# Optimization experiments

Hardware: AMD Instinct MI355X
Metric: run time of the kernel (lower is better)

Reference implementation:

```python
import jax, jax.numpy as jnp
import numpy as np

N_NODES = 50000
N_EDGES = 800000
D_FEAT = 128
HIDDEN = 128
OUT = 64
HEADS = 4


def setup_inputs() -> dict:
    key = jax.random.key(0)
    ks = jax.random.split(key, 12)
    s_in = 1.0 / np.sqrt(D_FEAT)
    s_h = 1.0 / np.sqrt(HIDDEN)
    x = jax.random.normal(ks[0], (N_NODES, D_FEAT), dtype=jnp.float32)
    edge_index = jax.random.randint(ks[1], (2, N_EDGES), 0, N_NODES, dtype=jnp.int32)
    return {
        "x": x,
        "edge_index": edge_index,
        # SAGEConv params: lin_l (aggregated neighbors), lin_r (root), bias
        "W_l": jax.random.normal(ks[2], (D_FEAT, HIDDEN), dtype=jnp.float32) * s_in,
        "W_r": jax.random.normal(ks[3], (D_FEAT, HIDDEN), dtype=jnp.float32) * s_in,
        "b_sage": jnp.zeros((HIDDEN,), dtype=jnp.float32),
        # GATConv params: lin_src, lin_dst (heads*hidden each), att vectors, bias
        "W_src": jax.random.normal(ks[4], (HIDDEN, HEADS * HIDDEN), dtype=jnp.float32) * s_h,
        "W_dst": jax.random.normal(ks[5], (HIDDEN, HEADS * HIDDEN), dtype=jnp.float32) * s_h,
        "att_src": jax.random.normal(ks[6], (HEADS, HIDDEN), dtype=jnp.float32) * s_h,
        "att_dst": jax.random.normal(ks[7], (HEADS, HIDDEN), dtype=jnp.float32) * s_h,
        "b_gat": jnp.zeros((HIDDEN,), dtype=jnp.float32),
        # Final Linear
        "W_lin": jax.random.normal(ks[8], (HIDDEN, OUT), dtype=jnp.float32) * s_h,
        "b_lin": jnp.zeros((OUT,), dtype=jnp.float32),
    }


def reference(x, edge_index, W_l, W_r, b_sage, W_src, W_dst, att_src, att_dst, b_gat, W_lin, b_lin):
    N = x.shape[0]
    src = edge_index[0]
    dst = edge_index[1]

    # ---- SAGEConv (mean aggregation): out = lin_l(mean_j x_j) + lin_r(x_i) + b ----
    agg = jax.ops.segment_sum(x[src], dst, num_segments=N)          # [N, d]
    cnt = jax.ops.segment_sum(jnp.ones_like(dst, dtype=x.dtype), dst, num_segments=N)
    mean_nbr = agg / jnp.maximum(cnt, 1.0)[:, None]
    h = mean_nbr @ W_l + x @ W_r + b_sage                           # [N, H*... no: [N, hidden]
    h = jax.nn.relu(h)

    # ---- GATConv (heads=4, concat=False -> mean over heads) ----
    H, C = att_src.shape
    hs = (h @ W_src).reshape(N, H, C)                               # source-transformed [N, H, C]
    hd = (h @ W_dst).reshape(N, H, C)                               # dest-transformed   [N, H, C]
    a_s = jnp.einsum('nhc,hc->nh', hs, att_src)                     # [N, H]
    a_d = jnp.einsum('nhc,hc->nh', hd, att_dst)                     # [N, H]
    e = jax.nn.leaky_relu(a_s[src] + a_d[dst], negative_slope=0.2)  # [E, H]
    # edge softmax over incoming edges per destination node
    e_max = jax.ops.segment_max(e, dst, num_segments=N)             # [N, H]
    e_exp = jnp.exp(e - e_max[dst])                                 # [E, H]
    denom = jax.ops.segment_sum(e_exp, dst, num_segments=N)         # [N, H]
    alpha = e_exp / denom[dst]                                      # [E, H]
    msg = hs[src] * alpha[:, :, None]                               # [E, H, C]
    out = jax.ops.segment_sum(msg, dst, num_segments=N)             # [N, H, C]
    out = out.mean(axis=1) + b_gat                                  # concat=False: avg heads
    out = jax.nn.relu(out)

    # ---- final Linear ----
    return out @ W_lin + b_lin
```

## Files before the change

### kernel.cpp

```cpp
#include <hip/hip_runtime.h>

#define D 128
#define HEADS 4

typedef __attribute__((ext_vector_type(8))) short short8;
typedef __attribute__((ext_vector_type(4))) float f32x4;

static __device__ __forceinline__ float leaky(float v) { return v > 0.f ? v : 0.2f * v; }

static __device__ __forceinline__ float2 bf2_to_f2(unsigned int u) {
    float2 r;
    union { unsigned int i; float f; } a, b;
    a.i = (u & 0xffffu) << 16;
    b.i = u & 0xffff0000u;
    r.x = a.f; r.y = b.f;
    return r;
}
static __device__ __forceinline__ float bf_to_f(unsigned short s) {
    union { unsigned int i; float f; } a;
    a.i = ((unsigned int)s) << 16;
    return a.f;
}
static __device__ __forceinline__ unsigned short f2bf(float f) {
    union { float f; unsigned int i; } v; v.f = f;
    unsigned int u = v.i;
    unsigned int r = (u + 0x7fffu + ((u >> 16) & 1u)) >> 16;
    return (unsigned short)r;
}

#define CPAD 16
#define HIST_BLOCKS 128
#define PREP_CNT 107520
#define MAXBUCK 2048
#define CH 8192

__global__ __launch_bounds__(256) void k_early(const float* __restrict__ x,
                                               const int* __restrict__ ei, int E, int npairs,
                                               const float* __restrict__ Wl, const float* __restrict__ Wr,
                                               const float* __restrict__ Wsrc, const float* __restrict__ Wlin,
                                               const float* __restrict__ Wdst,
                                               const float* __restrict__ atts, const float* __restrict__ attd,
                                               unsigned short* __restrict__ Bh,
                                               unsigned short* __restrict__ Bg,
                                               unsigned short* __restrict__ Bf,
                                               float* __restrict__ wsd,
                                               unsigned int* __restrict__ xb,
                                               int* __restrict__ bhist) {
    __shared__ int sh[MAXBUCK];
    int gb = blockIdx.x, t = threadIdx.x;
    if (gb < HIST_BLOCKS) {
        for (int i = t; i < MAXBUCK; i += 256) sh[i] = 0;
        __syncthreads();
        for (int i = gb * 256 + t; i < E; i += HIST_BLOCKS * 256)
            atomicAdd(&sh[ei[E + i] >> 5], 1);
        __syncthreads();
        for (int i = t; i < MAXBUCK; i += 256) if (sh[i]) atomicAdd(&bhist[i * CPAD], sh[i]);
        return;
    }
    int i = (gb - HIST_BLOCKS) * 256 + t;
    if (i < 32768) {
        int idx = i;
        int j = idx & 7, n16 = (idx >> 3) & 15, quad = (idx >> 7) & 3, rest = idx >> 9;
        int nc = rest & 7, kb = rest >> 3;
        int kk = kb * 32 + quad * 8 + j;
        int n = nc * 16 + n16;
        float v = (kk < 128) ? Wl[kk * 128 + n] : Wr[(kk - 128) * 128 + n];
        Bh[idx] = f2bf(v);
    } else if (i < 32768 + 65536) {
        int idx = i - 32768;
        int j = idx & 7, n16 = (idx >> 3) & 15, quad = (idx >> 7) & 3, rest = idx >> 9;
        int nc = rest & 7, kb = rest >> 3;
        int kk = kb * 32 + quad * 8 + j;
        int n = nc * 16 + n16;
        float v = Wsrc[(kk & 127) * 512 + (kk >> 7) * 128 + n];
        Bg[idx] = f2bf(v);
    } else if (i < 32768 + 65536 + 8192) {
        int idx = i - 98304;
        int j = idx & 7, n16 = (idx >> 3) & 15, quad = (idx >> 7) & 3, rest = idx >> 9;
        int nc = rest & 3, kb = rest >> 2;
        int kk = kb * 32 + quad * 8 + j;
        int n = nc * 16 + n16;
        Bf[idx] = f2bf(Wlin[kk * 64 + n]);
    } else if (i < PREP_CNT) {
        int tt = i - 106496;
        int k = tt >> 3, o = tt & 7;
        int hh = o & 3;
        const float* W = (o < 4) ? Wsrc : Wdst;
        const float* att = (o < 4) ? atts : attd;
        float acc = 0.f;
        for (int c = 0; c < 128; c++) acc += W[k * 512 + hh * 128 + c] * att[hh * 128 + c];
        wsd[k * 8 + o] = acc;
    } else {
        int p = i - PREP_CNT;
        if (p < npairs) {
            float2 v = *(const float2*)(x + (size_t)p * 2);
            xb[p] = (unsigned int)f2bf(v.x) | ((unsigned int)f2bf(v.y) << 16);
        }
    }
}

__global__ __launch_bounds__(256) void k_bscan(const int* __restrict__ bhist, int nbuck, int E,
                                               int* __restrict__ bbase, int* __restrict__ bcur,
                                               int* __restrict__ rowptr, int N) {
    __shared__ int ssum[256];
    int t = threadIdx.x;
    int base = t * 8;
    int v[8]; int s = 0;
    #pragma unroll
    for (int j = 0; j < 8; j++) {
        int idx = base + j;
        v[j] = (idx < nbuck) ? bhist[idx * CPAD] : 0;
        s += v[j];
    }
    ssum[t] = s;
    __syncthreads();
    for (int o = 1; o < 256; o <<= 1) {
        int tv = (t >= o) ? ssum[t - o] : 0;
        __syncthreads();
        ssum[t] += tv;
        __syncthreads();
    }
    int run = ssum[t] - s;
    #pragma unroll
    for (int j = 0; j < 8; j++) {
        int idx = base + j;
        if (idx < nbuck) { bbase[idx] = run; bcur[idx * CPAD] = run; }
        run += v[j];
    }
    if (t == 0) { bbase[nbuck] = E; rowptr[N] = E; }
}

__global__ __launch_bounds__(256) void k_scatter1(const int* __restrict__ ei, int E, int nbuck,
                                                  int* __restrict__ bcur,
                                                  unsigned int* __restrict__ ebuf) {
    __shared__ unsigned int sval[CH];
    __shared__ unsigned short soff[CH];
    __shared__ int cnt[MAXBUCK];
    __shared__ int gbase[MAXBUCK];
    int t = threadIdx.x;
    int c0 = blockIdx.x * CH;
    int ecnt = E - c0; if (ecnt > CH) ecnt = CH;
    for (int i = t; i < MAXBUCK; i += 256) cnt[i] = 0;
    __syncthreads();
    for (int i = t; i < ecnt; i += 256) {
        int s = ei[c0 + i], d = ei[E + c0 + i];
        int b = d >> 5;
        soff[i] = (unsigned short)atomicAdd(&cnt[b], 1);
        sval[i] = (unsigned int)s | ((unsigned int)(d & 31) << 16) | ((unsigned int)b << 21);
    }
    __syncthreads();
    for (int b = t; b < nbuck; b += 256)
        if (cnt[b]) gbase[b] = atomicAdd(&bcur[b * CPAD], cnt[b]);
    __syncthreads();
    for (int i = t; i < ecnt; i += 256) {
        unsigned int v = sval[i];
        int b = v >> 21;
        ebuf[gbase[b] + soff[i]] = v & 0x1fffffu;
    }
}

#define BCAP 1024
__global__ __launch_bounds__(256) void k_build_sage(const unsigned int* __restrict__ ebuf,
                                                    const int* __restrict__ bbase,
                                                    const unsigned int* __restrict__ xb,
                                                    int* __restrict__ csr,
                                                    int* __restrict__ rowptr,
                                                    unsigned int* __restrict__ meanb, int N) {
    __shared__ int cnt[32];
    __shared__ int excl[33];
    __shared__ unsigned char off[BCAP];
    __shared__ unsigned int rawv[BCAP];
    __shared__ int sorted[BCAP];
    int b = blockIdx.x, t = threadIdx.x;
    int e0 = bbase[b], e1 = bbase[b + 1];
    int ecnt = e1 - e0;
    if (ecnt > BCAP) ecnt = BCAP;
    if (t < 32) cnt[t] = 0;
    __syncthreads();
    for (int i = t; i < ecnt; i += 256) {
        unsigned int p = ebuf[e0 + i];
        rawv[i] = p;
        off[i] = (unsigned char)atomicAdd(&cnt[(p >> 16) & 31], 1);
    }
    __syncthreads();
    if (t == 0) {
        int run = 0;
        #pragma unroll
        for (int j = 0; j < 32; j++) { excl[j] = run; run += cnt[j]; }
        excl[32] = run;
    }
    __syncthreads();
    for (int i = t; i < ecnt; i += 256) {
        unsigned int p = rawv[i];
        int d = (p >> 16) & 31;
        sorted[excl[d] + off[i]] = (int)(p & 0xffffu);
    }
    __syncthreads();
    int nb0 = b << 5;
    if (t < 32 && nb0 + t < N) rowptr[nb0 + t] = e0 + excl[t];
    for (int i = t; i < ecnt; i += 256) csr[e0 + i] = sorted[i];
    int wv = t >> 6, lane = t & 63;
    for (int k = 0; k < 8; k++) {
        int local = wv * 8 + k;
        int node = nb0 + local;
        if (node >= N) continue;
        int le0 = excl[local], le1 = excl[local + 1];
        float ax = 0.f, ay = 0.f;
        int e = le0;
        for (; e + 3 < le1; e += 4) {
            int s0 = sorted[e], s1 = sorted[e + 1], s2 = sorted[e + 2], s3 = sorted[e + 3];
            unsigned int u0 = xb[(size_t)s0 * 64 + lane];
            unsigned int u1 = xb[(size_t)s1 * 64 + lane];
            unsigned int u2 = xb[(size_t)s2 * 64 + lane];
            unsigned int u3 = xb[(size_t)s3 * 64 + lane];
            float2 v0 = bf2_to_f2(u0), v1 = bf2_to_f2(u1), v2 = bf2_to_f2(u2), v3 = bf2_to_f2(u3);
            ax += (v0.x + v1.x) + (v2.x + v3.x);
            ay += (v0.y + v1.y) + (v2.y + v3.y);
        }
        for (; e < le1; e++) {
            float2 v0 = bf2_to_f2(xb[(size_t)sorted[e] * 64 + lane]);
            ax += v0.x; ay += v0.y;
        }
        int dg = le1 - le0;
        float inv = 1.0f / (float)(dg > 0 ? dg : 1);
        unsigned int o = (unsigned int)f2bf(ax * inv) | ((unsigned int)f2bf(ay * inv) << 16);
        __builtin_nontemporal_store(o, meanb + (size_t)node * 64 + lane);
    }
}

__global__ __launch_bounds__(256) void k_mfma_h(const unsigned short* __restrict__ A0,
                                                const unsigned short* __restrict__ A1,
                                                const unsigned short* __restrict__ Bp,
                                                const float* __restrict__ bias,
                                                const float* __restrict__ wsd,
                                                unsigned short* __restrict__ outb,
                                                float* __restrict__ a_s,
                                                float* __restrict__ a_d, int M) {
    const int NC = 8;
    __shared__ unsigned short sH[64][136];
    __shared__ float swsd[1024];
    int tid = threadIdx.x;
    int wave = tid >> 6;
    int lane = tid & 63;
    int row0 = blockIdx.x * 64 + wave * 16;
    int n16 = lane & 15, quad = lane >> 4;
    int arow = row0 + n16;
    int arowc = arow < M ? arow : 0;
    for (int i = tid; i < 1024; i += 256) swsd[i] = wsd[i];
    f32x4 acc[NC];
    #pragma unroll
    for (int i = 0; i < NC; i++) acc[i] = (f32x4){0.f, 0.f, 0.f, 0.f};
    #pragma unroll
    for (int kb = 0; kb < 8; kb++) {
        const unsigned short* ap = (kb < 4)
            ? (A0 + (size_t)arowc * 128 + kb * 32 + quad * 8)
            : (A1 + (size_t)arowc * 128 + (kb - 4) * 32 + quad * 8);
        short8 af = *(const short8*)ap;
        #pragma unroll
        for (int nc = 0; nc < NC; nc++) {
            short8 bf = *(const short8*)(Bp + ((((size_t)(kb * NC + nc) * 4 + quad) * 16 + n16) << 3));
            acc[nc] = __builtin_amdgcn_mfma_f32_16x16x32_bf16(af, bf, acc[nc], 0, 0, 0);
        }
    }
    int orow = row0 + quad * 4;
    int lrow = wave * 16 + quad * 4;
    #pragma unroll
    for (int r = 0; r < 4; r++) {
        int m = orow + r;
        #pragma unroll
        for (int nc = 0; nc < NC; nc++) {
            int col = nc * 16 + n16;
            float v = fmaxf(acc[nc][r] + bias[col], 0.f);
            unsigned short bv = f2bf(v);
            sH[lrow + r][col] = bv;
            if (m < M) outb[(size_t)m * 128 + col] = bv;
        }
    }
    __syncthreads();
    #pragma unroll
    for (int j = tid; j < 512; j += 256) {
        int m = j >> 3, o = j & 7;
        float accd = 0.f;
        #pragma unroll 4
        for (int k = 0; k < 128; k++)
            accd += bf_to_f(sH[m][k]) * swsd[k * 8 + o];
        int n = blockIdx.x * 64 + m;
        if (n < M) {
            if (o < 4) a_s[n * 4 + o] = accd;
            else       a_d[n * 4 + (o - 4)] = accd;
        }
    }
}

#define EDGE_CAP 192
__global__ __launch_bounds__(256) void k_gat_agg(const int* __restrict__ rowptr,
                                                 const int* __restrict__ csr,
                                                 const unsigned int* __restrict__ hb,
                                                 const float* __restrict__ a_s,
                                                 const float* __restrict__ a_d,
                                                 unsigned int* __restrict__ aggb, int N) {
    __shared__ int   sSrc[4][EDGE_CAP];
    __shared__ float sAl[4][EDGE_CAP * 4];
    int wv = threadIdx.x >> 6;
    int lane = threadIdx.x & 63;
    int n = blockIdx.x * 4 + wv;
    bool active = n < N;
    int e0 = 0, deg = 0;
    float4 ad = {0.f, 0.f, 0.f, 0.f};
    if (active) {
        e0 = rowptr[n];
        deg = rowptr[n + 1] - e0;
        ad = *(const float4*)(a_d + (size_t)n * 4);
    }
    f32x4 psum = {0.f, 0.f, 0.f, 0.f};
    for (int base = 0; base < deg; base += 64) {
        int i = base + lane;
        if (i < deg) {
            int s = csr[e0 + i];
            float4 as = *(const float4*)(a_s + (size_t)s * 4);
            f32x4 w;
            w.x = __expf(leaky(as.x + ad.x));
            w.y = __expf(leaky(as.y + ad.y));
            w.z = __expf(leaky(as.z + ad.z));
            w.w = __expf(leaky(as.w + ad.w));
            psum += w;
            if (i < EDGE_CAP) {
                sSrc[wv][i] = s;
                *(f32x4*)&sAl[wv][i * 4] = w;
            }
        }
    }
    #pragma unroll
    for (int o = 32; o; o >>= 1) {
        psum.x += __shfl_xor(psum.x, o);
        psum.y += __shfl_xor(psum.y, o);
        psum.z += __shfl_xor(psum.z, o);
        psum.w += __shfl_xor(psum.w, o);
    }
    f32x4 inv;
    inv.x = psum.x > 0.f ? 0.25f / psum.x : 0.f;
    inv.y = psum.y > 0.f ? 0.25f / psum.y : 0.f;
    inv.z = psum.z > 0.f ? 0.25f / psum.z : 0.f;
    inv.w = psum.w > 0.f ? 0.25f / psum.w : 0.f;
    int capdeg = deg < EDGE_CAP ? deg : EDGE_CAP;
    for (int base = 0; base < capdeg; base += 64) {
        int i = base + lane;
        if (i < capdeg) {
            f32x4 w = *(f32x4*)&sAl[wv][i * 4];
            w *= inv;
            *(f32x4*)&sAl[wv][i * 4] = w;
        }
    }
    __syncthreads();
    float2 ac0 = {0, 0}, ac1 = {0, 0}, ac2 = {0, 0}, ac3 = {0, 0};
    int e = 0;
    for (; e + 3 < capdeg; e += 4) {
        int s0 = sSrc[wv][e], s1 = sSrc[wv][e + 1], s2 = sSrc[wv][e + 2], s3 = sSrc[wv][e + 3];
        f32x4 w0 = *(const f32x4*)&sAl[wv][e * 4];
        f32x4 w1 = *(const f32x4*)&sAl[wv][e * 4 + 4];
        f32x4 w2 = *(const f32x4*)&sAl[wv][e * 4 + 8];
        f32x4 w3 = *(const f32x4*)&sAl[wv][e * 4 + 12];
        unsigned int u0 = hb[(size_t)s0 * 64 + lane];
        unsigned int u1 = hb[(size_t)s1 * 64 + lane];
        unsigned int u2 = hb[(size_t)s2 * 64 + lane];
        unsigned int u3 = hb[(size_t)s3 * 64 + lane];
        float2 v0 = bf2_to_f2(u0), v1 = bf2_to_f2(u1), v2 = bf2_to_f2(u2), v3 = bf2_to_f2(u3);
        ac0.x += w0.x * v0.x + w1.x * v1.x + w2.x * v2.x + w3.x * v3.x;
        ac0.y += w0.x * v0.y + w1.x * v1.y + w2.x * v2.y + w3.x * v3.y;
        ac1.x += w0.y * v0.x + w1.y * v1.x + w2.y * v2.x + w3.y * v3.x;
        ac1.y += w0.y * v0.y + w1.y * v1.y + w2.y * v2.y + w3.y * v3.y;
        ac2.x += w0.z * v0.x + w1.z * v1.x + w2.z * v2.x + w3.z * v3.x;
        ac2.y += w0.z * v0.y + w1.z * v1.y + w2.z * v2.y + w3.z * v3.y;
        ac3.x += w0.w * v0.x + w1.w * v1.x + w2.w * v2.x + w3.w * v3.x;
        ac3.y += w0.w * v0.y + w1.w * v1.y + w2.w * v2.y + w3.w * v3.y;
    }
    for (; e < capdeg; e++) {
        int s0 = sSrc[wv][e];
        f32x4 w0 = *(const f32x4*)&sAl[wv][e * 4];
        unsigned int u0 = hb[(size_t)s0 * 64 + lane];
        float2 v0 = bf2_to_f2(u0);
        ac0.x += w0.x * v0.x; ac0.y += w0.x * v0.y;
        ac1.x += w0.y * v0.x; ac1.y += w0.y * v0.y;
        ac2.x += w0.z * v0.x; ac2.y += w0.z * v0.y;
        ac3.x += w0.w * v0.x; ac3.y += w0.w * v0.y;
    }
    for (int i = EDGE_CAP; i < deg; i++) {
        int s = csr[e0 + i];
        float4 as = *(const float4*)(a_s + (size_t)s * 4);
        f32x4 w;
        w.x = __expf(leaky(as.x + ad.x)) * inv.x;
        w.y = __expf(leaky(as.y + ad.y)) * inv.y;
        w.z = __expf(leaky(as.z + ad.z)) * inv.z;
        w.w = __expf(leaky(as.w + ad.w)) * inv.w;
        float2 v0 = bf2_to_f2(hb[(size_t)s * 64 + lane]);
        ac0.x += w.x * v0.x; ac0.y += w.x * v0.y;
        ac1.x += w.y * v0.x; ac1.y += w.y * v0.y;
        ac2.x += w.z * v0.x; ac2.y += w.z * v0.y;
        ac3.x += w.w * v0.x; ac3.y += w.w * v0.y;
    }
    if (!active) return;
    unsigned int* rowu = aggb + (size_t)n * 256 + lane;
    unsigned int o0 = (unsigned int)f2bf(ac0.x) | ((unsigned int)f2bf(ac0.y) << 16);
    unsigned int o1 = (unsigned int)f2bf(ac1.x) | ((unsigned int)f2bf(ac1.y) << 16);
    unsigned int o2 = (unsigned int)f2bf(ac2.x) | ((unsigned int)f2bf(ac2.y) << 16);
    unsigned int o3 = (unsigned int)f2bf(ac3.x) | ((unsigned int)f2bf(ac3.y) << 16);
    __builtin_nontemporal_store(o0, rowu + 0);
    __builtin_nontemporal_store(o1, rowu + 64);
    __builtin_nontemporal_store(o2, rowu + 128);
    __builtin_nontemporal_store(o3, rowu + 192);
}

__global__ __launch_bounds__(256) void k_mfma_tail(const unsigned short* __restrict__ aggb,
                                                   const unsigned short* __restrict__ Bg,
                                                   const float* __restrict__ bg,
                                                   const unsigned short* __restrict__ Bf,
                                                   const float* __restrict__ bl,
                                                   float* __restrict__ out, int M) {
    __shared__ unsigned short sG[64][136];
    int wave = threadIdx.x >> 6;
    int lane = threadIdx.x & 63;
    int row0 = blockIdx.x * 64 + wave * 16;
    int n16 = lane & 15, quad = lane >> 4;
    {
        int arow = row0 + n16;
        int arowc = arow < M ? arow : 0;
        const unsigned short* ap = aggb + (size_t)arowc * 512 + quad * 8;
        f32x4 acc[8];
        #pragma unroll
        for (int i = 0; i < 8; i++) acc[i] = (f32x4){0.f, 0.f, 0.f, 0.f};
        #pragma unroll
        for (int kb = 0; kb < 16; kb++) {
            short8 af = *(const short8*)(ap + kb * 32);
            #pragma unroll
            for (int nc = 0; nc < 8; nc++) {
                short8 bf = *(const short8*)(Bg + ((((size_t)(kb * 8 + nc) * 4 + quad) * 16 + n16) << 3));
                acc[nc] = __builtin_amdgcn_mfma_f32_16x16x32_bf16(af, bf, acc[nc], 0, 0, 0);
            }
        }
        int lrow = wave * 16 + quad * 4;
        #pragma unroll
        for (int r = 0; r < 4; r++) {
            #pragma unroll
            for (int nc = 0; nc < 8; nc++) {
                int col = nc * 16 + n16;
                sG[lrow + r][col] = f2bf(fmaxf(acc[nc][r] + bg[col], 0.f));
            }
        }
    }
    __syncthreads();
    {
        f32x4 acc[4];
        #pragma unroll
        for (int i = 0; i < 4; i++) acc[i] = (f32x4){0.f, 0.f, 0.f, 0.f};
        #pragma unroll
        for (int kb = 0; kb < 4; kb++) {
            short8 af = *(const short8*)&sG[wave * 16 + n16][kb * 32 + quad * 8];
            #pragma unroll
            for (int nc = 0; nc < 4; nc++) {
                short8 bf = *(const short8*)(Bf + ((((size_t)(kb * 4 + nc) * 4 + quad) * 16 + n16) << 3));
                acc[nc] = __builtin_amdgcn_mfma_f32_16x16x32_bf16(af, bf, acc[nc], 0, 0, 0);
            }
        }
        int orow = row0 + quad * 4;
        #pragma unroll
        for (int r = 0; r < 4; r++) {
            int m = orow + r;
            if (m < M) {
                #pragma unroll
                for (int nc = 0; nc < 4; nc++) {
                    int col = nc * 16 + n16;
                    out[(size_t)m * 64 + col] = acc[nc][r] + bl[col];
                }
            }
        }
    }
}

extern "C" void kernel_launch(void* const* d_in, const int* in_sizes, int n_in,
                              void* d_out, int out_size, void* d_ws, size_t ws_size,
                              hipStream_t stream) {
    const float* x    = (const float*)d_in[0];
    const int*   ei   = (const int*)d_in[1];
    const float* Wl   = (const float*)d_in[2];
    const float* Wr   = (const float*)d_in[3];
    const float* bs   = (const float*)d_in[4];
    const float* Wsrc = (const float*)d_in[5];
    const float* Wdst = (const float*)d_in[6];
    const float* atts = (const float*)d_in[7];
    const float* attd = (const float*)d_in[8];
    const float* bg   = (const float*)d_in[9];
    const float* Wlin = (const float*)d_in[10];
    const float* bl   = (const float*)d_in[11];
    int N = in_sizes[0] / D;
    int E = in_sizes[1] / 2;
    int nbuck = (N + 31) >> 5;
    int npairs = N * 64;

    char* w = (char*)d_ws;
    auto alloc = [&](size_t bytes) {
        char* p = w;
        w += (bytes + 255) & ~(size_t)255;
        return p;
    };
    unsigned int* xb     = (unsigned int*)alloc((size_t)N * 256);
    unsigned int* meanb  = (unsigned int*)alloc((size_t)N * 256);
    unsigned int* hb     = (unsigned int*)alloc((size_t)N * 256);
    unsigned int* aggb   = (unsigned int*)alloc((size_t)N * 1024);
    unsigned short* Bh   = (unsigned short*)alloc(65536 * 2);
    unsigned short* Bg   = (unsigned short*)alloc(65536 * 2);
    unsigned short* Bf   = (unsigned short*)alloc(8192 * 2);
    float* a_s           = (float*)alloc((size_t)N * 16);
    float* a_d           = (float*)alloc((size_t)N * 16);
    float* wsd           = (float*)alloc(1024 * 4);
    int* rowptr          = (int*)alloc((size_t)(N + 64) * 4);
    int* bhist           = (int*)alloc((size_t)MAXBUCK * CPAD * 4);
    int* bbase           = (int*)alloc((size_t)(MAXBUCK + 1) * 4);
    int* bcur            = (int*)alloc((size_t)MAXBUCK * CPAD * 4);
    unsigned int* ebuf   = (unsigned int*)alloc((size_t)E * 4);
    int* csr             = (int*)alloc((size_t)E * 4);
    (void)ws_size; (void)n_in; (void)out_size;

    hipMemsetAsync(bhist, 0, (size_t)MAXBUCK * CPAD * 4, stream);

    int workBlocks = (PREP_CNT + npairs + 255) / 256;
    k_early<<<HIST_BLOCKS + workBlocks, 256, 0, stream>>>(x, ei, E, npairs,
                                                          Wl, Wr, Wsrc, Wlin, Wdst, atts, attd,
                                                          Bh, Bg, Bf, wsd, xb, bhist);
    k_bscan<<<1, 256, 0, stream>>>(bhist, nbuck, E, bbase, bcur, rowptr, N);
    k_scatter1<<<(E + CH - 1) / CH, 256, 0, stream>>>(ei, E, nbuck, bcur, ebuf);
    k_build_sage<<<nbuck, 256, 0, stream>>>(ebuf, bbase, xb, csr, rowptr, meanb, N);

    k_mfma_h<<<(N + 63) / 64, 256, 0, stream>>>((const unsigned short*)meanb,
                                                (const unsigned short*)xb, Bh, bs, wsd,
                                                (unsigned short*)hb, a_s, a_d, N);
    k_gat_agg<<<(N + 3) / 4, 256, 0, stream>>>(rowptr, csr, hb, a_s, a_d, aggb, N);
    k_mfma_tail<<<(N + 63) / 64, 256, 0, stream>>>((const unsigned short*)aggb, Bg, bg,
                                                   Bf, bl, (float*)d_out, N);
}
```

Baseline: 270.0 us.

## Replace bucket histogram and scan with fixed-capacity bucket slots; widen GAT gather

Each destination bucket now gets a fixed slot of 1024 edges, so the scatter kernel writes to `b<<10` plus an atomic offset. This removes the histogram pass over edges in `k_early` and the single-block scan kernel. Row extents become explicit `rowptr`/`rowend` arrays instead of a prefix-summed `rowptr`. The GAT aggregation stores precomputed byte offsets in shared memory, unrolls the gather by 8 to keep more loads in flight, and drops a block-wide barrier that guarded only wave-private shared data. Buckets with more than 1024 incoming edges would silently lose edges, and the edge and CSR buffers grow to a padded size.

New measurement: 260.0 us. 3.7% less time.

```diff
diff --git a/kernel.cpp b/kernel.cpp
--- a/kernel.cpp
+++ b/kernel.cpp
@@ -29,13 +29,12 @@
 }
 
 #define CPAD 16
-#define HIST_BLOCKS 128
 #define PREP_CNT 107520
 #define MAXBUCK 2048
+#define BSLOT 1024
 #define CH 8192
 
-__global__ __launch_bounds__(256) void k_early(const float* __restrict__ x,
-                                               const int* __restrict__ ei, int E, int npairs,
+__global__ __launch_bounds__(256) void k_early(const float* __restrict__ x, int npairs,
                                                const float* __restrict__ Wl, const float* __restrict__ Wr,
                                                const float* __restrict__ Wsrc, const float* __restrict__ Wlin,
                                                const float* __restrict__ Wdst,
@@ -44,20 +43,8 @@
                                                unsigned short* __restrict__ Bg,
                                                unsigned short* __restrict__ Bf,
                                                float* __restrict__ wsd,
-                                               unsigned int* __restrict__ xb,
-                                               int* __restrict__ bhist) {
-    __shared__ int sh[MAXBUCK];
-    int gb = blockIdx.x, t = threadIdx.x;
-    if (gb < HIST_BLOCKS) {
-        for (int i = t; i < MAXBUCK; i += 256) sh[i] = 0;
-        __syncthreads();
-        for (int i = gb * 256 + t; i < E; i += HIST_BLOCKS * 256)
-            atomicAdd(&sh[ei[E + i] >> 5], 1);
-        __syncthreads();
-        for (int i = t; i < MAXBUCK; i += 256) if (sh[i]) atomicAdd(&bhist[i * CPAD], sh[i]);
-        return;
-    }
-    int i = (gb - HIST_BLOCKS) * 256 + t;
+                                               unsigned int* __restrict__ xb) {
+    int i = blockIdx.x * 256 + threadIdx.x;
     if (i < 32768) {
         int idx = i;
         int j = idx & 7, n16 = (idx >> 3) & 15, quad = (idx >> 7) & 3, rest = idx >> 9;
@@ -99,37 +86,6 @@
     }
 }
 
-__global__ __launch_bounds__(256) void k_bscan(const int* __restrict__ bhist, int nbuck, int E,
-                                               int* __restrict__ bbase, int* __restrict__ bcur,
-                                               int* __restrict__ rowptr, int N) {
-    __shared__ int ssum[256];
-    int t = threadIdx.x;
-    int base = t * 8;
-    int v[8]; int s = 0;
-    #pragma unroll
-    for (int j = 0; j < 8; j++) {
-        int idx = base + j;
-        v[j] = (idx < nbuck) ? bhist[idx * CPAD] : 0;
-        s += v[j];
-    }
-    ssum[t] = s;
-    __syncthreads();
-    for (int o = 1; o < 256; o <<= 1) {
-        int tv = (t >= o) ? ssum[t - o] : 0;
-        __syncthreads();
-        ssum[t] += tv;
-        __syncthreads();
-    }
-    int run = ssum[t] - s;
-    #pragma unroll
-    for (int j = 0; j < 8; j++) {
-        int idx = base + j;
-        if (idx < nbuck) { bbase[idx] = run; bcur[idx * CPAD] = run; }
-        run += v[j];
-    }
-    if (t == 0) { bbase[nbuck] = E; rowptr[N] = E; }
-}
-
 __global__ __launch_bounds__(256) void k_scatter1(const int* __restrict__ ei, int E, int nbuck,
                                                   int* __restrict__ bcur,
                                                   unsigned int* __restrict__ ebuf) {
@@ -150,21 +106,23 @@
     }
     __syncthreads();
     for (int b = t; b < nbuck; b += 256)
-        if (cnt[b]) gbase[b] = atomicAdd(&bcur[b * CPAD], cnt[b]);
+        if (cnt[b]) gbase[b] = (b << 10) + atomicAdd(&bcur[b * CPAD], cnt[b]);
     __syncthreads();
     for (int i = t; i < ecnt; i += 256) {
         unsigned int v = sval[i];
         int b = v >> 21;
-        ebuf[gbase[b] + soff[i]] = v & 0x1fffffu;
+        int pos = gbase[b] + soff[i];
+        if (pos < ((b + 1) << 10)) ebuf[pos] = v & 0x1fffffu;
     }
 }
 
 #define BCAP 1024
 __global__ __launch_bounds__(256) void k_build_sage(const unsigned int* __restrict__ ebuf,
-                                                    const int* __restrict__ bbase,
+                                                    const int* __restrict__ bcur,
                                                     const unsigned int* __restrict__ xb,
                                                     int* __restrict__ csr,
                                                     int* __restrict__ rowptr,
+                                                    int* __restrict__ rowend,
                                                     unsigned int* __restrict__ meanb, int N) {
     __shared__ int cnt[32];
     __shared__ int excl[33];
@@ -172,8 +130,8 @@
     __shared__ unsigned int rawv[BCAP];
     __shared__ int sorted[BCAP];
     int b = blockIdx.x, t = threadIdx.x;
-    int e0 = bbase[b], e1 = bbase[b + 1];
-    int ecnt = e1 - e0;
+    int e0 = b << 10;
+    int ecnt = bcur[b * CPAD];
     if (ecnt > BCAP) ecnt = BCAP;
     if (t < 32) cnt[t] = 0;
     __syncthreads();
@@ -197,7 +155,10 @@
     }
     __syncthreads();
     int nb0 = b << 5;
-    if (t < 32 && nb0 + t < N) rowptr[nb0 + t] = e0 + excl[t];
+    if (t < 32 && nb0 + t < N) {
+        rowptr[nb0 + t] = e0 + excl[t];
+        rowend[nb0 + t] = e0 + excl[t + 1];
+    }
     for (int i = t; i < ecnt; i += 256) csr[e0 + i] = sorted[i];
     int wv = t >> 6, lane = t & 63;
     for (int k = 0; k < 8; k++) {
@@ -294,12 +255,13 @@
 
 #define EDGE_CAP 192
 __global__ __launch_bounds__(256) void k_gat_agg(const int* __restrict__ rowptr,
+                                                 const int* __restrict__ rowend,
                                                  const int* __restrict__ csr,
                                                  const unsigned int* __restrict__ hb,
                                                  const float* __restrict__ a_s,
                                                  const float* __restrict__ a_d,
                                                  unsigned int* __restrict__ aggb, int N) {
-    __shared__ int   sSrc[4][EDGE_CAP];
+    __shared__ int   sOff[4][EDGE_CAP];
     __shared__ float sAl[4][EDGE_CAP * 4];
     int wv = threadIdx.x >> 6;
     int lane = threadIdx.x & 63;
@@ -309,7 +271,7 @@
     float4 ad = {0.f, 0.f, 0.f, 0.f};
     if (active) {
         e0 = rowptr[n];
-        deg = rowptr[n + 1] - e0;
+        deg = rowend[n] - e0;
         ad = *(const float4*)(a_d + (size_t)n * 4);
     }
     f32x4 psum = {0.f, 0.f, 0.f, 0.f};
@@ -325,7 +287,7 @@
             w.w = __expf(leaky(as.w + ad.w));
             psum += w;
             if (i < EDGE_CAP) {
-                sSrc[wv][i] = s;
+                sOff[wv][i] = s << 8;
                 *(f32x4*)&sAl[wv][i * 4] = w;
             }
         }
@@ -351,33 +313,42 @@
             *(f32x4*)&sAl[wv][i * 4] = w;
         }
     }
-    __syncthreads();
+    const char* hbL = (const char*)hb + lane * 4;
     float2 ac0 = {0, 0}, ac1 = {0, 0}, ac2 = {0, 0}, ac3 = {0, 0};
     int e = 0;
+    for (; e + 7 < capdeg; e += 8) {
+        unsigned int u[8];
+        #pragma unroll
+        for (int q = 0; q < 8; q++)
+            u[q] = *(const unsigned int*)(hbL + sOff[wv][e + q]);
+        #pragma unroll
+        for (int q = 0; q < 8; q++) {
+            f32x4 w = *(const f32x4*)&sAl[wv][(e + q) * 4];
+            float2 v = bf2_to_f2(u[q]);
+            ac0.x += w.x * v.x; ac0.y += w.x * v.y;
+            ac1.x += w.y * v.x; ac1.y += w.y * v.y;
+            ac2.x += w.z * v.x; ac2.y += w.z * v.y;
+            ac3.x += w.w * v.x; ac3.y += w.w * v.y;
+        }
+    }
     for (; e + 3 < capdeg; e += 4) {
-        int s0 = sSrc[wv][e], s1 = sSrc[wv][e + 1], s2 = sSrc[wv][e + 2], s3 = sSrc[wv][e + 3];
+        unsigned int u[4];
+        #pragma unroll
+        for (int q = 0; q < 4; q++)
+            u[q] = *(const unsigned int*)(hbL + sOff[wv][e + q]);
+        #pragma unroll
+        for (int q = 0; q < 4; q++) {
+            f32x4 w = *(const f32x4*)&sAl[wv][(e + q) * 4];
+            float2 v = bf2_to_f2(u[q]);
+            ac0.x += w.x * v.x; ac0.y += w.x * v.y;
+            ac1.x += w.y * v.x; ac1.y += w.y * v.y;
+            ac2.x += w.z * v.x; ac2.y += w.z * v.y;
+            ac3.x += w.w * v.x; ac3.y += w.w * v.y;
+        }
+    }
+    for (; e < capdeg; e++) {
+        unsigned int u0 = *(const unsigned int*)(hbL + sOff[wv][e]);
         f32x4 w0 = *(const f32x4*)&sAl[wv][e * 4];
-        f32x4 w1 = *(const f32x4*)&sAl[wv][e * 4 + 4];
-        f32x4 w2 = *(const f32x4*)&sAl[wv][e * 4 + 8];
-        f32x4 w3 = *(const f32x4*)&sAl[wv][e * 4 + 12];
-        unsigned int u0 = hb[(size_t)s0 * 64 + lane];
-        unsigned int u1 = hb[(size_t)s1 * 64 + lane];
-        unsigned int u2 = hb[(size_t)s2 * 64 + lane];
-        unsigned int u3 = hb[(size_t)s3 * 64 + lane];
-        float2 v0 = bf2_to_f2(u0), v1 = bf2_to_f2(u1), v2 = bf2_to_f2(u2), v3 = bf2_to_f2(u3);
-        ac0.x += w0.x * v0.x + w1.x * v1.x + w2.x * v2.x + w3.x * v3.x;
-        ac0.y += w0.x * v0.y + w1.x * v1.y + w2.x * v2.y + w3.x * v3.y;
-        ac1.x += w0.y * v0.x + w1.y * v1.x + w2.y * v2.x + w3.y * v3.x;
-        ac1.y += w0.y * v0.y + w1.y * v1.y + w2.y * v2.y + w3.y * v3.y;
-        ac2.x += w0.z * v0.x + w1.z * v1.x + w2.z * v2.x + w3.z * v3.x;
-        ac2.y += w0.z * v0.y + w1.z * v1.y + w2.z * v2.y + w3.z * v3.y;
-        ac3.x += w0.w * v0.x + w1.w * v1.x + w2.w * v2.x + w3.w * v3.x;
-        ac3.y += w0.w * v0.y + w1.w * v1.y + w2.w * v2.y + w3.w * v3.y;
-    }
-    for (; e < capdeg; e++) {
-        int s0 = sSrc[wv][e];
-        f32x4 w0 = *(const f32x4*)&sAl[wv][e * 4];
-        unsigned int u0 = hb[(size_t)s0 * 64 + lane];
         float2 v0 = bf2_to_f2(u0);
         ac0.x += w0.x * v0.x; ac0.y += w0.x * v0.y;
         ac1.x += w0.y * v0.x; ac1.y += w0.y * v0.y;
@@ -512,28 +483,25 @@
     float* a_s           = (float*)alloc((size_t)N * 16);
     float* a_d           = (float*)alloc((size_t)N * 16);
     float* wsd           = (float*)alloc(1024 * 4);
-    int* rowptr          = (int*)alloc((size_t)(N + 64) * 4);
-    int* bhist           = (int*)alloc((size_t)MAXBUCK * CPAD * 4);
-    int* bbase           = (int*)alloc((size_t)(MAXBUCK + 1) * 4);
+    int* rowptr          = (int*)alloc((size_t)N * 4);
+    int* rowend          = (int*)alloc((size_t)N * 4);
     int* bcur            = (int*)alloc((size_t)MAXBUCK * CPAD * 4);
-    unsigned int* ebuf   = (unsigned int*)alloc((size_t)E * 4);
-    int* csr             = (int*)alloc((size_t)E * 4);
+    unsigned int* ebuf   = (unsigned int*)alloc((size_t)MAXBUCK * BSLOT * 4);
+    int* csr             = (int*)alloc((size_t)MAXBUCK * BSLOT * 4);
     (void)ws_size; (void)n_in; (void)out_size;
 
-    hipMemsetAsync(bhist, 0, (size_t)MAXBUCK * CPAD * 4, stream);
+    hipMemsetAsync(bcur, 0, (size_t)MAXBUCK * CPAD * 4, stream);
 
     int workBlocks = (PREP_CNT + npairs + 255) / 256;
-    k_early<<<HIST_BLOCKS + workBlocks, 256, 0, stream>>>(x, ei, E, npairs,
-                                                          Wl, Wr, Wsrc, Wlin, Wdst, atts, attd,
-                                                          Bh, Bg, Bf, wsd, xb, bhist);
-    k_bscan<<<1, 256, 0, stream>>>(bhist, nbuck, E, bbase, bcur, rowptr, N);
+    k_early<<<workBlocks, 256, 0, stream>>>(x, npairs, Wl, Wr, Wsrc, Wlin, Wdst, atts, attd,
+                                            Bh, Bg, Bf, wsd, xb);
     k_scatter1<<<(E + CH - 1) / CH, 256, 0, stream>>>(ei, E, nbuck, bcur, ebuf);
-    k_build_sage<<<nbuck, 256, 0, stream>>>(ebuf, bbase, xb, csr, rowptr, meanb, N);
+    k_build_sage<<<nbuck, 256, 0, stream>>>(ebuf, bcur, xb, csr, rowptr, rowend, meanb, N);
 
     k_mfma_h<<<(N + 63) / 64, 256, 0, stream>>>((const unsigned short*)meanb,
                                                 (const unsigned short*)xb, Bh, bs, wsd,
                                                 (unsigned short*)hb, a_s, a_d, N);
-    k_gat_agg<<<(N + 3) / 4, 256, 0, stream>>>(rowptr, csr, hb, a_s, a_d, aggb, N);
+    k_gat_agg<<<(N + 3) / 4, 256, 0, stream>>>(rowptr, rowend, csr, hb, a_s, a_d, aggb, N);
     k_mfma_tail<<<(N + 63) / 64, 256, 0, stream>>>((const unsigned short*)aggb, Bg, bg,
                                                    Bf, bl, (float*)d_out, N);
 }
```
